# Optimization experiments

Measured on AMD Instinct MI355X. Metric: run time of the kernel, lower is better.

## Reference

```python
import jax, jax.numpy as jnp
import numpy as np

B, C, H, W = 8, 64, 16, 16
TE = 128      # te_hidden
GT = 256      # rn_gt_hidden
FP = 256      # rn_fp_hidden
A = 32        # a_size
O = H * W
PAIR_IN = (C + 2) * 2 + TE  # 260, matches (cv_filter+2)*2 + te_hidden


def setup_inputs() -> dict:
    key = jax.random.key(0)
    ks = jax.random.split(key, 10)

    def w(k, fan_in, fan_out):
        return (jax.random.normal(k, (fan_in, fan_out), jnp.float32)
                / np.sqrt(fan_in).astype(np.float32))

    return {
        "x": jax.random.normal(ks[0], (B, C, H, W), jnp.float32),
        "code": jax.random.normal(ks[1], (B, TE), jnp.float32),
        "gt_w1": w(ks[2], PAIR_IN, GT), "gt_b1": jnp.zeros((GT,), jnp.float32),
        "gt_w2": w(ks[3], GT, GT),      "gt_b2": jnp.zeros((GT,), jnp.float32),
        "gt_w3": w(ks[4], GT, GT),      "gt_b3": jnp.zeros((GT,), jnp.float32),
        "fp_w1": w(ks[5], GT, FP),      "fp_b1": jnp.zeros((FP,), jnp.float32),
        "fp_w2": w(ks[6], FP, FP),      "fp_b2": jnp.zeros((FP,), jnp.float32),
        "fp_w3": w(ks[7], FP, A),       "fp_b3": jnp.zeros((A,), jnp.float32),
    }


def _coords(h, w):
    # 2 normalized coordinate channels in [-1, 1], one value per object
    ys = jnp.linspace(-1.0, 1.0, h, dtype=jnp.float32)
    xs = jnp.linspace(-1.0, 1.0, w, dtype=jnp.float32)
    yy, xx = jnp.meshgrid(ys, xs, indexing="ij")
    return jnp.stack([yy.ravel(), xx.ravel()], axis=-1)  # (o, 2)


def reference(x, code, gt_w1, gt_b1, gt_w2, gt_b2, gt_w3, gt_b3,
              fp_w1, fp_b1, fp_w2, fp_b2, fp_w3, fp_b3):
    b, c, h, w = x.shape
    o = h * w
    te = code.shape[-1]

    # rn_encode: flatten spatial grid to objects, append 2 coord channels
    xo = x.reshape(b, c, o).transpose(0, 2, 1)                 # (b, o, c)
    coord = jnp.broadcast_to(_coords(h, w)[None], (b, o, 2))
    xo = jnp.concatenate([xo, coord], axis=-1)                 # (b, o, c+2)

    # all O^2 ordered pairs + broadcast question code
    xi = jnp.broadcast_to(xo[:, :, None, :], (b, o, o, c + 2))
    xj = jnp.broadcast_to(xo[:, None, :, :], (b, o, o, c + 2))
    q = jnp.broadcast_to(code[:, None, None, :], (b, o, o, te))
    pairs = jnp.concatenate([xi, xj, q], axis=-1)              # (b, o, o, PAIR_IN)

    # g_theta MLP (ReLU after every layer)
    h1 = jax.nn.relu(pairs @ gt_w1 + gt_b1)
    h2 = jax.nn.relu(h1 @ gt_w2 + gt_b2)
    rel = jax.nn.relu(h2 @ gt_w3 + gt_b3)                      # (b, o, o, GT)

    # lower_sum: sum relations over the lower-triangular (i >= j) pairs
    mask = jnp.tril(jnp.ones((o, o), rel.dtype))
    summed = jnp.einsum("bijd,ij->bd", rel, mask)              # (b, GT)

    # f_phi MLP; no activation on final logits, dropout=0 (eval)
    f1 = jax.nn.relu(summed @ fp_w1 + fp_b1)
    f2 = jax.nn.relu(f1 @ fp_w2 + fp_b2)
    logits = f2 @ fp_w3 + fp_b3                                # (b, A)
    return logits
```

## Files before the change

kernel.cpp:

```cpp
#include <hip/hip_runtime.h>
#include <stdint.h>


#define NPAIR 32896
#define NPT   129

using short8  = __attribute__((ext_vector_type(8))) short;
using float4v = __attribute__((ext_vector_type(4))) float;

__device__ __forceinline__ float asf(unsigned u) {
    union { unsigned u; float f; } c; c.u = u; return c.f;
}
__device__ __forceinline__ unsigned short f2bf(float f) {
    union { float f; unsigned u; } c; c.f = f;
    unsigned u = c.u;
    u += 0x7FFFu + ((u >> 16) & 1u);
    return (unsigned short)(u >> 16);
}
__device__ __forceinline__ unsigned cvtpk(float lo, float hi) {
    unsigned r;
    asm("v_cvt_pk_bf16_f32 %0, %1, %2" : "=v"(r) : "v"(lo), "v"(hi));
    return r;
}
__device__ __forceinline__ void ij_of(int p, int& i, int& j) {
    float s = sqrtf(8.0f * (float)p + 1.0f);
    i = (int)((s - 1.0f) * 0.5f);
    while ((i + 1) * (i + 2) / 2 <= p) ++i;
    while (i * (i + 1) / 2 > p) --i;
    j = p - i * (i + 1) / 2;
}
__device__ __forceinline__ short8 buildA(uint4 uu, uint4 vv) {
    unsigned ua[4] = {uu.x, uu.y, uu.z, uu.w};
    unsigned va[4] = {vv.x, vv.y, vv.z, vv.w};
    union { unsigned u[4]; short8 s; } c;
    #pragma unroll
    for (int q = 0; q < 4; ++q) {
        float lo = asf(ua[q] << 16)         + asf(va[q] << 16);
        float hi = asf(ua[q] & 0xFFFF0000u) + asf(va[q] & 0xFFFF0000u);
        c.u[q] = cvtpk(fmaxf(lo, 0.f), fmaxf(hi, 0.f));
    }
    return c.s;
}

__global__ __launch_bounds__(256) void k_pre(
    const float* __restrict__ x, const float* __restrict__ code,
    const float* __restrict__ w1, const float* __restrict__ b1,
    const float* __restrict__ w2, const float* __restrict__ w3,
    unsigned short* __restrict__ ub, unsigned short* __restrict__ vb,
    unsigned short* __restrict__ w2t, unsigned short* __restrict__ w3t,
    float* __restrict__ summed)
{
    const int tid = threadIdx.x;
    if (blockIdx.x < 32) {
        const int ig = blockIdx.x, b = blockIdx.y, d = tid;
        float q = b1[d];
        const float* cp = code + b * 128;
        #pragma unroll 16
        for (int t = 0; t < 128; ++t) q += cp[t] * w1[(132 + t) * 256 + d];
        float su[8], sv[8];
        #pragma unroll
        for (int k = 0; k < 8; ++k) { su[k] = q; sv[k] = 0.f; }
        const float* xp = x + (b * 64) * 256 + ig * 8;
        #pragma unroll 8
        for (int c = 0; c < 64; ++c) {
            const float wu = w1[c * 256 + d];
            const float wv = w1[(66 + c) * 256 + d];
            const float* xc = xp + c * 256;
            #pragma unroll
            for (int k = 0; k < 8; ++k) { su[k] += xc[k] * wu; sv[k] += xc[k] * wv; }
        }
        const float wyu = w1[64 * 256 + d],  wxu = w1[65 * 256 + d];
        const float wyv = w1[130 * 256 + d], wxv = w1[131 * 256 + d];
        #pragma unroll
        for (int k = 0; k < 8; ++k) {
            const int i = ig * 8 + k;
            const float yy = (float)(i >> 4) * (2.0f / 15.0f) - 1.0f;
            const float xx = (float)(i & 15) * (2.0f / 15.0f) - 1.0f;
            ub[(b * 256 + i) * 256 + d] = f2bf(su[k] + yy * wyu + xx * wxu);
            vb[(b * 256 + i) * 256 + d] = f2bf(sv[k] + yy * wyv + xx * wxv);
        }
    } else {
        __shared__ float t[64][65];
        const int y = blockIdx.y;
        summed[y * 256 + tid] = 0.f;
        const int tx = tid & 63, ty = tid >> 6;
        for (int jj = 0; jj < 4; ++jj) {
            const int job = y * 4 + jj;
            const float* src = (job & 16) ? w3 : w2;
            unsigned short* dst = (job & 16) ? w3t : w2t;
            const int k0 = ((job >> 2) & 3) * 64, n0 = (job & 3) * 64;
            __syncthreads();
            #pragma unroll
            for (int r = ty; r < 64; r += 4) t[r][tx] = src[(k0 + r) * 256 + n0 + tx];
            __syncthreads();
            #pragma unroll
            for (int r = ty; r < 64; r += 4) dst[(n0 + r) * 256 + k0 + tx] = f2bf(t[tx][r]);
        }
    }
}

__global__ __launch_bounds__(512) void k_fuse(
    const unsigned short* __restrict__ ub, const unsigned short* __restrict__ vb,
    const unsigned short* __restrict__ w2t, const unsigned short* __restrict__ w3t,
    const float* __restrict__ b2, const float* __restrict__ b3,
    float* __restrict__ summed)
{
    extern __shared__ unsigned short lds[];
    const int tid  = threadIdx.x;
    const int pt   = blockIdx.x, b = blockIdx.y;
    const int lane = tid & 63, w = tid >> 6;
    const int lm   = lane & 15, quad = lane >> 4;

    #pragma unroll
    for (int it = 0; it < 16; ++it) {
        const int idx = it * 512 + tid;
        const int n = idx >> 5, c = idx & 31;
        const uint4 d = *(const uint4*)(w2t + n * 256 + c * 8);
        *(uint4*)(&lds[n * 256 + ((c ^ (n & 7)) << 3)]) = d;
    }

    const unsigned short* up[2];
    const unsigned short* vp[2];
    #pragma unroll
    for (int mt = 0; mt < 2; ++mt) {
        const int p0 = pt * 256 + w * 32 + mt * 16 + lm;
        const int p  = p0 < NPAIR ? p0 : NPAIR - 1;
        int i, j; ij_of(p, i, j);
        up[mt] = ub + ((b * 256 + i) * 256) + quad * 8;
        vp[mt] = vb + ((b * 256 + j) * 256) + quad * 8;
    }
    const int wave_valid = (pt * 256 + w * 32) < NPAIR;
    __syncthreads();

    const float4v zero4 = {0.f, 0.f, 0.f, 0.f};

    float4v acc1[16][2];
    #pragma unroll
    for (int nt = 0; nt < 16; ++nt)
        #pragma unroll
        for (int mt = 0; mt < 2; ++mt) acc1[nt][mt] = zero4;
    {
        uint4 cu[3][2], cv[3][2];
        #pragma unroll
        for (int kk = 0; kk < 3; ++kk)
            #pragma unroll
            for (int mt = 0; mt < 2; ++mt) {
                cu[kk][mt] = *(const uint4*)(up[mt] + kk * 32);
                cv[kk][mt] = *(const uint4*)(vp[mt] + kk * 32);
            }
        #pragma unroll
        for (int ks = 0; ks < 8; ++ks) {
            const int pr = ks % 3;
            short8 afr[2];
            #pragma unroll
            for (int mt = 0; mt < 2; ++mt) afr[mt] = buildA(cu[pr][mt], cv[pr][mt]);
            if (ks < 5) {
                #pragma unroll
                for (int mt = 0; mt < 2; ++mt) {
                    cu[pr][mt] = *(const uint4*)(up[mt] + (ks + 3) * 32);
                    cv[pr][mt] = *(const uint4*)(vp[mt] + (ks + 3) * 32);
                }
            }
            const int coff = ((ks * 4 + quad) ^ (lm & 7)) << 3;
            __builtin_amdgcn_s_setprio(1);
            #pragma unroll
            for (int ng = 0; ng < 4; ++ng) {
                short8 bfr[4];
                #pragma unroll
                for (int q = 0; q < 4; ++q)
                    bfr[q] = *(const short8*)(&lds[((ng * 4 + q) * 16 + lm) * 256 + coff]);
                #pragma unroll
                for (int q = 0; q < 4; ++q)
                    #pragma unroll
                    for (int mt = 0; mt < 2; ++mt)
                        acc1[ng * 4 + q][mt] = __builtin_amdgcn_mfma_f32_16x16x32_bf16(
                            bfr[q], afr[mt], acc1[ng * 4 + q][mt], 0, 0, 0);
            }
            __builtin_amdgcn_s_setprio(0);
        }
    }
    __syncthreads();

    const unsigned short* bb3 = w3t + ((w * 32 + lm) * 256) + quad * 8;
    short8 bbuf[2][2];
    #pragma unroll
    for (int kk = 0; kk < 2; ++kk)
        #pragma unroll
        for (int nt = 0; nt < 2; ++nt)
            bbuf[kk][nt] = *(const short8*)(bb3 + nt * 4096 + kk * 32);

    const float msk = wave_valid ? 1.f : 0.f;
    #pragma unroll
    for (int nt = 0; nt < 16; ++nt) {
        const float4 bbv = *(const float4*)(b2 + nt * 16 + quad * 4);
        #pragma unroll
        for (int mt = 0; mt < 2; ++mt) {
            const int row = w * 32 + mt * 16 + lm;
            const float v0 = fmaxf(acc1[nt][mt][0] + bbv.x, 0.f) * msk;
            const float v1 = fmaxf(acc1[nt][mt][1] + bbv.y, 0.f) * msk;
            const float v2 = fmaxf(acc1[nt][mt][2] + bbv.z, 0.f) * msk;
            const float v3 = fmaxf(acc1[nt][mt][3] + bbv.w, 0.f) * msk;
            uint2 pk; pk.x = cvtpk(v0, v1); pk.y = cvtpk(v2, v3);
            const int c0 = nt * 2 + (quad >> 1);
            *(uint2*)(&lds[row * 256 + (((c0 ^ (row & 7)) << 3) | ((quad & 1) << 2))]) = pk;
        }
    }
    __syncthreads();

    float4v acc2[16][2];
    #pragma unroll
    for (int mt = 0; mt < 16; ++mt)
        #pragma unroll
        for (int nt = 0; nt < 2; ++nt) acc2[mt][nt] = zero4;
    {
        for (int ks = 0; ks < 8; ++ks) {
            const int pr = ks & 1;
            short8 bcur[2];
            #pragma unroll
            for (int nt = 0; nt < 2; ++nt) bcur[nt] = bbuf[pr][nt];
            if (ks < 6) {
                #pragma unroll
                for (int nt = 0; nt < 2; ++nt)
                    bbuf[pr][nt] = *(const short8*)(bb3 + nt * 4096 + (ks + 2) * 32);
            }
            __builtin_amdgcn_s_setprio(1);
            #pragma unroll
            for (int mt = 0; mt < 16; ++mt) {
                const int row = mt * 16 + lm;
                const short8 a = *(const short8*)(
                    &lds[row * 256 + (((ks * 4 + quad) ^ (row & 7)) << 3)]);
                #pragma unroll
                for (int nt = 0; nt < 2; ++nt)
                    acc2[mt][nt] = __builtin_amdgcn_mfma_f32_16x16x32_bf16(
                        a, bcur[nt], acc2[mt][nt], 0, 0, 0);
            }
            __builtin_amdgcn_s_setprio(0);
        }
    }

    #pragma unroll
    for (int nt = 0; nt < 2; ++nt) {
        const int col = w * 32 + nt * 16 + lm;
        const float bb = b3[col];
        float s = 0.f;
        #pragma unroll
        for (int mt = 0; mt < 16; ++mt)
            #pragma unroll
            for (int rg = 0; rg < 4; ++rg)
                s += fmaxf(acc2[mt][nt][rg] + bb, 0.f);
        s += __shfl_xor(s, 16);
        s += __shfl_xor(s, 32);
        if (quad == 0)
            atomicAdd(&summed[b * 256 + col], s);
    }
}

__global__ __launch_bounds__(1024) void k_tail(
    const float* __restrict__ summed,
    const float* __restrict__ fw1, const float* __restrict__ fb1,
    const float* __restrict__ fw2, const float* __restrict__ fb2,
    const float* __restrict__ fw3, const float* __restrict__ fb3,
    float* __restrict__ out)
{
    __shared__ float s0[256], s1[256], red[1024];
    const int b = blockIdx.x, tid = threadIdx.x;
    const int d = tid & 255, kh = tid >> 8;
    if (tid < 256) s0[tid] = summed[b * 256 + tid];
    __syncthreads();
    float p = 0.f;
    #pragma unroll 16
    for (int k = kh * 64; k < kh * 64 + 64; ++k) p += s0[k] * fw1[k * 256 + d];
    red[kh * 256 + d] = p;
    __syncthreads();
    if (tid < 256)
        s1[tid] = fmaxf(red[tid] + red[256 + tid] + red[512 + tid] + red[768 + tid]
                        + fb1[tid], 0.f);
    __syncthreads();
    p = 0.f;
    #pragma unroll 16
    for (int k = kh * 64; k < kh * 64 + 64; ++k) p += s1[k] * fw2[k * 256 + d];
    red[kh * 256 + d] = p;
    __syncthreads();
    if (tid < 256)
        s0[tid] = fmaxf(red[tid] + red[256 + tid] + red[512 + tid] + red[768 + tid]
                        + fb2[tid], 0.f);
    __syncthreads();
    const int d3 = tid & 31, kh3 = tid >> 5;
    p = 0.f;
    #pragma unroll
    for (int k = kh3 * 8; k < kh3 * 8 + 8; ++k) p += s0[k] * fw3[k * 32 + d3];
    red[kh3 * 32 + d3] = p;
    __syncthreads();
    if (tid < 32) {
        float o = fb3[tid];
        #pragma unroll 8
        for (int r = 0; r < 32; ++r) o += red[r * 32 + tid];
        out[b * 32 + tid] = o;
    }
}

extern "C" void kernel_launch(void* const* d_in, const int* in_sizes, int n_in,
                              void* d_out, int out_size, void* d_ws, size_t ws_size,
                              hipStream_t stream) {
    const float* x    = (const float*)d_in[0];
    const float* code = (const float*)d_in[1];
    const float* gw1  = (const float*)d_in[2];
    const float* gb1  = (const float*)d_in[3];
    const float* gw2  = (const float*)d_in[4];
    const float* gb2  = (const float*)d_in[5];
    const float* gw3  = (const float*)d_in[6];
    const float* gb3  = (const float*)d_in[7];
    const float* fw1  = (const float*)d_in[8];
    const float* fb1  = (const float*)d_in[9];
    const float* fw2  = (const float*)d_in[10];
    const float* fb2  = (const float*)d_in[11];
    const float* fw3  = (const float*)d_in[12];
    const float* fb3  = (const float*)d_in[13];
    float* out = (float*)d_out;

    char* ws = (char*)d_ws;
    unsigned short* ub  = (unsigned short*)(ws);
    unsigned short* vb  = (unsigned short*)(ws + 1048576);
    unsigned short* w2t = (unsigned short*)(ws + 2097152);
    unsigned short* w3t = (unsigned short*)(ws + 2228224);
    float* summed = (float*)(ws + 2359296);

    hipLaunchKernelGGL(k_pre, dim3(33, 8), dim3(256), 0, stream,
                       x, code, gw1, gb1, gw2, gw3, ub, vb, w2t, w3t, summed);
    hipLaunchKernelGGL(k_fuse, dim3(NPT, 8), dim3(512), 131072, stream,
                       ub, vb, w2t, w3t, gb2, gb3, summed);
    hipLaunchKernelGGL(k_tail, dim3(8), dim3(1024), 0, stream,
                       summed, fw1, fb1, fw2, fb2, fw3, fb3, out);
}
```

Before: 192.2 us.

## Stage pair activations in LDS and stream W2 fragments per wave

The fused g_theta kernel now builds the 128-pair layer-1 activation tile in LDS, with a swizzled layout. Each wave streams its own 32-column slice of W2 from global memory, mirroring how W3 was already handled. Previously all of W2 was staged in LDS and activations were built in registers. The tile size halves to 128 pairs, so LDS use drops to 64KB and more blocks can be resident per CU. The 257 tiles cover the pairs exactly, so the validity masking is removed. The trade-off is more global/L2 reads of weight fragments and twice as many blocks.

New measurement: 210.5 us. 9.5% more time.

```diff
diff --git a/kernel.cpp b/kernel.cpp
--- a/kernel.cpp
+++ b/kernel.cpp
@@ -3,7 +3,7 @@
 
 
 #define NPAIR 32896
-#define NPT   129
+#define NTILE 257
 
 using short8  = __attribute__((ext_vector_type(8))) short;
 using float4v = __attribute__((ext_vector_type(4))) float;
@@ -29,17 +29,18 @@
     while (i * (i + 1) / 2 > p) --i;
     j = p - i * (i + 1) / 2;
 }
-__device__ __forceinline__ short8 buildA(uint4 uu, uint4 vv) {
+__device__ __forceinline__ uint4 build4(uint4 uu, uint4 vv) {
     unsigned ua[4] = {uu.x, uu.y, uu.z, uu.w};
     unsigned va[4] = {vv.x, vv.y, vv.z, vv.w};
-    union { unsigned u[4]; short8 s; } c;
+    uint4 r;
+    unsigned* rp = (unsigned*)&r;
     #pragma unroll
     for (int q = 0; q < 4; ++q) {
         float lo = asf(ua[q] << 16)         + asf(va[q] << 16);
         float hi = asf(ua[q] & 0xFFFF0000u) + asf(va[q] & 0xFFFF0000u);
-        c.u[q] = cvtpk(fmaxf(lo, 0.f), fmaxf(hi, 0.f));
-    }
-    return c.s;
+        rp[q] = cvtpk(fmaxf(lo, 0.f), fmaxf(hi, 0.f));
+    }
+    return r;
 }
 
 __global__ __launch_bounds__(256) void k_pre(
@@ -99,117 +100,112 @@
     }
 }
 
-__global__ __launch_bounds__(512) void k_fuse(
+__global__ __launch_bounds__(512, 4) void k_fuse(
     const unsigned short* __restrict__ ub, const unsigned short* __restrict__ vb,
     const unsigned short* __restrict__ w2t, const unsigned short* __restrict__ w3t,
     const float* __restrict__ b2, const float* __restrict__ b3,
     float* __restrict__ summed)
 {
-    extern __shared__ unsigned short lds[];
+    extern __shared__ unsigned short tile[];
     const int tid  = threadIdx.x;
     const int pt   = blockIdx.x, b = blockIdx.y;
     const int lane = tid & 63, w = tid >> 6;
     const int lm   = lane & 15, quad = lane >> 4;
 
-    #pragma unroll
-    for (int it = 0; it < 16; ++it) {
-        const int idx = it * 512 + tid;
-        const int n = idx >> 5, c = idx & 31;
-        const uint4 d = *(const uint4*)(w2t + n * 256 + c * 8);
-        *(uint4*)(&lds[n * 256 + ((c ^ (n & 7)) << 3)]) = d;
-    }
-
-    const unsigned short* up[2];
-    const unsigned short* vp[2];
-    #pragma unroll
-    for (int mt = 0; mt < 2; ++mt) {
-        const int p0 = pt * 256 + w * 32 + mt * 16 + lm;
-        const int p  = p0 < NPAIR ? p0 : NPAIR - 1;
+    const unsigned short* bb2 = w2t + ((w * 32 + lm) * 256) + quad * 8;
+    const unsigned short* bb3 = w3t + ((w * 32 + lm) * 256) + quad * 8;
+
+    short8 bbuf[2][2];
+    #pragma unroll
+    for (int kk = 0; kk < 2; ++kk)
+        #pragma unroll
+        for (int nt = 0; nt < 2; ++nt)
+            bbuf[kk][nt] = *(const short8*)(bb2 + nt * 4096 + kk * 32);
+
+    {
+        const int r = tid >> 2, qq = tid & 3;
+        const int p = pt * 128 + r;
         int i, j; ij_of(p, i, j);
-        up[mt] = ub + ((b * 256 + i) * 256) + quad * 8;
-        vp[mt] = vb + ((b * 256 + j) * 256) + quad * 8;
-    }
-    const int wave_valid = (pt * 256 + w * 32) < NPAIR;
+        const unsigned short* up = ub + ((b * 256 + i) * 256) + qq * 64;
+        const unsigned short* vp = vb + ((b * 256 + j) * 256) + qq * 64;
+        const int rs = r & 7;
+        #pragma unroll
+        for (int it = 0; it < 8; ++it) {
+            const uint4 uu = *(const uint4*)(up + it * 8);
+            const uint4 vv = *(const uint4*)(vp + it * 8);
+            const uint4 r4 = build4(uu, vv);
+            const int chunk = qq * 8 + it;
+            *(uint4*)(&tile[r * 256 + ((chunk ^ rs) << 3)]) = r4;
+        }
+    }
     __syncthreads();
 
     const float4v zero4 = {0.f, 0.f, 0.f, 0.f};
 
-    float4v acc1[16][2];
-    #pragma unroll
-    for (int nt = 0; nt < 16; ++nt)
-        #pragma unroll
-        for (int mt = 0; mt < 2; ++mt) acc1[nt][mt] = zero4;
+    float4v acc1[2][8];
+    #pragma unroll
+    for (int nt = 0; nt < 2; ++nt)
+        #pragma unroll
+        for (int mt = 0; mt < 8; ++mt) acc1[nt][mt] = zero4;
     {
-        uint4 cu[3][2], cv[3][2];
-        #pragma unroll
-        for (int kk = 0; kk < 3; ++kk)
-            #pragma unroll
-            for (int mt = 0; mt < 2; ++mt) {
-                cu[kk][mt] = *(const uint4*)(up[mt] + kk * 32);
-                cv[kk][mt] = *(const uint4*)(vp[mt] + kk * 32);
-            }
-        #pragma unroll
         for (int ks = 0; ks < 8; ++ks) {
-            const int pr = ks % 3;
-            short8 afr[2];
-            #pragma unroll
-            for (int mt = 0; mt < 2; ++mt) afr[mt] = buildA(cu[pr][mt], cv[pr][mt]);
-            if (ks < 5) {
-                #pragma unroll
-                for (int mt = 0; mt < 2; ++mt) {
-                    cu[pr][mt] = *(const uint4*)(up[mt] + (ks + 3) * 32);
-                    cv[pr][mt] = *(const uint4*)(vp[mt] + (ks + 3) * 32);
-                }
+            const int pr = ks & 1;
+            short8 bcur[2];
+            #pragma unroll
+            for (int nt = 0; nt < 2; ++nt) bcur[nt] = bbuf[pr][nt];
+            if (ks < 6) {
+                #pragma unroll
+                for (int nt = 0; nt < 2; ++nt)
+                    bbuf[pr][nt] = *(const short8*)(bb2 + nt * 4096 + (ks + 2) * 32);
             }
             const int coff = ((ks * 4 + quad) ^ (lm & 7)) << 3;
             __builtin_amdgcn_s_setprio(1);
             #pragma unroll
-            for (int ng = 0; ng < 4; ++ng) {
-                short8 bfr[4];
-                #pragma unroll
-                for (int q = 0; q < 4; ++q)
-                    bfr[q] = *(const short8*)(&lds[((ng * 4 + q) * 16 + lm) * 256 + coff]);
-                #pragma unroll
-                for (int q = 0; q < 4; ++q)
+            for (int half = 0; half < 2; ++half) {
+                short8 afr[4];
+                #pragma unroll
+                for (int m = 0; m < 4; ++m)
+                    afr[m] = *(const short8*)(
+                        &tile[((half * 4 + m) * 16 + lm) * 256 + coff]);
+                #pragma unroll
+                for (int m = 0; m < 4; ++m)
                     #pragma unroll
-                    for (int mt = 0; mt < 2; ++mt)
-                        acc1[ng * 4 + q][mt] = __builtin_amdgcn_mfma_f32_16x16x32_bf16(
-                            bfr[q], afr[mt], acc1[ng * 4 + q][mt], 0, 0, 0);
+                    for (int nt = 0; nt < 2; ++nt)
+                        acc1[nt][half * 4 + m] = __builtin_amdgcn_mfma_f32_16x16x32_bf16(
+                            bcur[nt], afr[m], acc1[nt][half * 4 + m], 0, 0, 0);
             }
             __builtin_amdgcn_s_setprio(0);
         }
     }
     __syncthreads();
 
-    const unsigned short* bb3 = w3t + ((w * 32 + lm) * 256) + quad * 8;
-    short8 bbuf[2][2];
     #pragma unroll
     for (int kk = 0; kk < 2; ++kk)
         #pragma unroll
         for (int nt = 0; nt < 2; ++nt)
             bbuf[kk][nt] = *(const short8*)(bb3 + nt * 4096 + kk * 32);
 
-    const float msk = wave_valid ? 1.f : 0.f;
-    #pragma unroll
-    for (int nt = 0; nt < 16; ++nt) {
-        const float4 bbv = *(const float4*)(b2 + nt * 16 + quad * 4);
-        #pragma unroll
-        for (int mt = 0; mt < 2; ++mt) {
-            const int row = w * 32 + mt * 16 + lm;
-            const float v0 = fmaxf(acc1[nt][mt][0] + bbv.x, 0.f) * msk;
-            const float v1 = fmaxf(acc1[nt][mt][1] + bbv.y, 0.f) * msk;
-            const float v2 = fmaxf(acc1[nt][mt][2] + bbv.z, 0.f) * msk;
-            const float v3 = fmaxf(acc1[nt][mt][3] + bbv.w, 0.f) * msk;
+    #pragma unroll
+    for (int nt = 0; nt < 2; ++nt) {
+        const float4 bbv = *(const float4*)(b2 + w * 32 + nt * 16 + quad * 4);
+        #pragma unroll
+        for (int mt = 0; mt < 8; ++mt) {
+            const int row = mt * 16 + lm;
+            const float v0 = fmaxf(acc1[nt][mt][0] + bbv.x, 0.f);
+            const float v1 = fmaxf(acc1[nt][mt][1] + bbv.y, 0.f);
+            const float v2 = fmaxf(acc1[nt][mt][2] + bbv.z, 0.f);
+            const float v3 = fmaxf(acc1[nt][mt][3] + bbv.w, 0.f);
             uint2 pk; pk.x = cvtpk(v0, v1); pk.y = cvtpk(v2, v3);
-            const int c0 = nt * 2 + (quad >> 1);
-            *(uint2*)(&lds[row * 256 + (((c0 ^ (row & 7)) << 3) | ((quad & 1) << 2))]) = pk;
-        }
-    }
-    __syncthreads();
-
-    float4v acc2[16][2];
-    #pragma unroll
-    for (int mt = 0; mt < 16; ++mt)
+            const int c0 = w * 4 + nt * 2 + (quad >> 1);
+            *(uint2*)(&tile[row * 256 +
+                            (((c0 ^ (row & 7)) << 3) | ((quad & 1) << 2))]) = pk;
+        }
+    }
+    __syncthreads();
+
+    float4v acc2[8][2];
+    #pragma unroll
+    for (int mt = 0; mt < 8; ++mt)
         #pragma unroll
         for (int nt = 0; nt < 2; ++nt) acc2[mt][nt] = zero4;
     {
@@ -223,12 +219,12 @@
                 for (int nt = 0; nt < 2; ++nt)
                     bbuf[pr][nt] = *(const short8*)(bb3 + nt * 4096 + (ks + 2) * 32);
             }
+            const int coff = ((ks * 4 + quad) ^ (lm & 7)) << 3;
             __builtin_amdgcn_s_setprio(1);
             #pragma unroll
-            for (int mt = 0; mt < 16; ++mt) {
-                const int row = mt * 16 + lm;
+            for (int mt = 0; mt < 8; ++mt) {
                 const short8 a = *(const short8*)(
-                    &lds[row * 256 + (((ks * 4 + quad) ^ (row & 7)) << 3)]);
+                    &tile[(mt * 16 + lm) * 256 + coff]);
                 #pragma unroll
                 for (int nt = 0; nt < 2; ++nt)
                     acc2[mt][nt] = __builtin_amdgcn_mfma_f32_16x16x32_bf16(
@@ -244,7 +240,7 @@
         const float bb = b3[col];
         float s = 0.f;
         #pragma unroll
-        for (int mt = 0; mt < 16; ++mt)
+        for (int mt = 0; mt < 8; ++mt)
             #pragma unroll
             for (int rg = 0; rg < 4; ++rg)
                 s += fmaxf(acc2[mt][nt][rg] + bb, 0.f);
@@ -327,7 +323,7 @@
 
     hipLaunchKernelGGL(k_pre, dim3(33, 8), dim3(256), 0, stream,
                        x, code, gw1, gb1, gw2, gw3, ub, vb, w2t, w3t, summed);
-    hipLaunchKernelGGL(k_fuse, dim3(NPT, 8), dim3(512), 131072, stream,
+    hipLaunchKernelGGL(k_fuse, dim3(NTILE, 8), dim3(512), 65536, stream,
                        ub, vb, w2t, w3t, gb2, gb3, summed);
     hipLaunchKernelGGL(k_tail, dim3(8), dim3(1024), 0, stream,
                        summed, fw1, fb1, fw2, fb2, fw3, fb3, out);
```

## Move ragged last pair tile from fused kernel into tail kernel

Applied to the files above, without the earlier changes.

The main fused kernel now launches 128 pair tiles per batch instead of 129, dropping the mostly-empty 129th tile (128 valid pairs out of 256) and its masking logic. The tail kernel processes the remaining 128 pairs itself with a smaller MFMA pass before the f_phi MLP, adding its partial sum to the accumulated relations. This removes a nearly idle extra wave of blocks on the main kernel, but the single-block-per-batch tail kernel now does extra serial work and needs about 135 KB of dynamic LDS.

Result: faster. 187.7 us (-2.3%).

```diff
diff --git a/kernel.cpp b/kernel.cpp
--- a/kernel.cpp
+++ b/kernel.cpp
@@ -3,7 +3,6 @@
 
 
 #define NPAIR 32896
-#define NPT   129
 
 using short8  = __attribute__((ext_vector_type(8))) short;
 using float4v = __attribute__((ext_vector_type(4))) float;
@@ -123,13 +122,11 @@
     const unsigned short* vp[2];
     #pragma unroll
     for (int mt = 0; mt < 2; ++mt) {
-        const int p0 = pt * 256 + w * 32 + mt * 16 + lm;
-        const int p  = p0 < NPAIR ? p0 : NPAIR - 1;
+        const int p = pt * 256 + w * 32 + mt * 16 + lm;
         int i, j; ij_of(p, i, j);
         up[mt] = ub + ((b * 256 + i) * 256) + quad * 8;
         vp[mt] = vb + ((b * 256 + j) * 256) + quad * 8;
     }
-    const int wave_valid = (pt * 256 + w * 32) < NPAIR;
     __syncthreads();
 
     const float4v zero4 = {0.f, 0.f, 0.f, 0.f};
@@ -189,17 +186,16 @@
         for (int nt = 0; nt < 2; ++nt)
             bbuf[kk][nt] = *(const short8*)(bb3 + nt * 4096 + kk * 32);
 
-    const float msk = wave_valid ? 1.f : 0.f;
     #pragma unroll
     for (int nt = 0; nt < 16; ++nt) {
         const float4 bbv = *(const float4*)(b2 + nt * 16 + quad * 4);
         #pragma unroll
         for (int mt = 0; mt < 2; ++mt) {
             const int row = w * 32 + mt * 16 + lm;
-            const float v0 = fmaxf(acc1[nt][mt][0] + bbv.x, 0.f) * msk;
-            const float v1 = fmaxf(acc1[nt][mt][1] + bbv.y, 0.f) * msk;
-            const float v2 = fmaxf(acc1[nt][mt][2] + bbv.z, 0.f) * msk;
-            const float v3 = fmaxf(acc1[nt][mt][3] + bbv.w, 0.f) * msk;
+            const float v0 = fmaxf(acc1[nt][mt][0] + bbv.x, 0.f);
+            const float v1 = fmaxf(acc1[nt][mt][1] + bbv.y, 0.f);
+            const float v2 = fmaxf(acc1[nt][mt][2] + bbv.z, 0.f);
+            const float v3 = fmaxf(acc1[nt][mt][3] + bbv.w, 0.f);
             uint2 pk; pk.x = cvtpk(v0, v1); pk.y = cvtpk(v2, v3);
             const int c0 = nt * 2 + (quad >> 1);
             *(uint2*)(&lds[row * 256 + (((c0 ^ (row & 7)) << 3) | ((quad & 1) << 2))]) = pk;
@@ -256,40 +252,143 @@
 }
 
 __global__ __launch_bounds__(1024) void k_tail(
+    const unsigned short* __restrict__ ub, const unsigned short* __restrict__ vb,
+    const unsigned short* __restrict__ w2t, const unsigned short* __restrict__ w3t,
+    const float* __restrict__ b2, const float* __restrict__ b3,
     const float* __restrict__ summed,
     const float* __restrict__ fw1, const float* __restrict__ fb1,
     const float* __restrict__ fw2, const float* __restrict__ fb2,
     const float* __restrict__ fw3, const float* __restrict__ fb3,
     float* __restrict__ out)
 {
-    __shared__ float s0[256], s1[256], red[1024];
+    extern __shared__ unsigned short lds[];
+    float* ext = (float*)(lds + 65536);
+    float* s0  = ext + 256;
+    float* s1  = s0 + 256;
+    float* red = s1 + 256;
     const int b = blockIdx.x, tid = threadIdx.x;
+    const int lane = tid & 63, w = tid >> 6;
+    const int lm = lane & 15, quad = lane >> 4;
+    const float4v zero4 = {0.f, 0.f, 0.f, 0.f};
+
+    #pragma unroll
+    for (int it = 0; it < 8; ++it) {
+        const int idx = it * 1024 + tid;
+        const int n = idx >> 5, c = idx & 31;
+        const uint4 d4 = *(const uint4*)(w2t + n * 256 + c * 8);
+        *(uint4*)(&lds[n * 256 + ((c ^ (n & 7)) << 3)]) = d4;
+    }
+    const int pp = 32768 + w * 16 + lm;
+    const int p  = pp < NPAIR ? pp : NPAIR - 1;
+    int i, j; ij_of(p, i, j);
+    const unsigned short* up = ub + ((b * 256 + i) * 256) + quad * 8;
+    const unsigned short* vp = vb + ((b * 256 + j) * 256) + quad * 8;
+    __syncthreads();
+
+    float4v acc1[16];
+    #pragma unroll
+    for (int nt = 0; nt < 16; ++nt) acc1[nt] = zero4;
+    if (tid < 512) {
+        #pragma unroll
+        for (int ks = 0; ks < 8; ++ks) {
+            const uint4 cu = *(const uint4*)(up + ks * 32);
+            const uint4 cv = *(const uint4*)(vp + ks * 32);
+            const short8 afr = buildA(cu, cv);
+            const int coff = ((ks * 4 + quad) ^ (lm & 7)) << 3;
+            #pragma unroll
+            for (int nt = 0; nt < 16; ++nt) {
+                const short8 bfr = *(const short8*)(&lds[(nt * 16 + lm) * 256 + coff]);
+                acc1[nt] = __builtin_amdgcn_mfma_f32_16x16x32_bf16(
+                    bfr, afr, acc1[nt], 0, 0, 0);
+            }
+        }
+    }
+    __syncthreads();
+
+    if (tid < 512) {
+        #pragma unroll
+        for (int nt = 0; nt < 16; ++nt) {
+            const float4 bbv = *(const float4*)(b2 + nt * 16 + quad * 4);
+            const int row = w * 16 + lm;
+            const float v0 = fmaxf(acc1[nt][0] + bbv.x, 0.f);
+            const float v1 = fmaxf(acc1[nt][1] + bbv.y, 0.f);
+            const float v2 = fmaxf(acc1[nt][2] + bbv.z, 0.f);
+            const float v3 = fmaxf(acc1[nt][3] + bbv.w, 0.f);
+            uint2 pk; pk.x = cvtpk(v0, v1); pk.y = cvtpk(v2, v3);
+            const int c0 = nt * 2 + (quad >> 1);
+            *(uint2*)(&lds[row * 256 + (((c0 ^ (row & 7)) << 3) | ((quad & 1) << 2))]) = pk;
+        }
+    }
+    __syncthreads();
+
+    float4v acc2[8][2];
+    #pragma unroll
+    for (int mt = 0; mt < 8; ++mt)
+        #pragma unroll
+        for (int nt = 0; nt < 2; ++nt) acc2[mt][nt] = zero4;
+    if (tid < 512) {
+        const unsigned short* bb3 = w3t + ((w * 32 + lm) * 256) + quad * 8;
+        #pragma unroll
+        for (int ks = 0; ks < 8; ++ks) {
+            short8 bcur[2];
+            #pragma unroll
+            for (int nt = 0; nt < 2; ++nt)
+                bcur[nt] = *(const short8*)(bb3 + nt * 4096 + ks * 32);
+            const int coff = ((ks * 4 + quad) ^ (lm & 7)) << 3;
+            #pragma unroll
+            for (int mt = 0; mt < 8; ++mt) {
+                const int row = mt * 16 + lm;
+                const short8 a = *(const short8*)(
+                    &lds[row * 256 + (((ks * 4 + quad) ^ (row & 7)) << 3)]);
+                #pragma unroll
+                for (int nt = 0; nt < 2; ++nt)
+                    acc2[mt][nt] = __builtin_amdgcn_mfma_f32_16x16x32_bf16(
+                        a, bcur[nt], acc2[mt][nt], 0, 0, 0);
+            }
+        }
+        #pragma unroll
+        for (int nt = 0; nt < 2; ++nt) {
+            const int col = w * 32 + nt * 16 + lm;
+            const float bb = b3[col];
+            float s = 0.f;
+            #pragma unroll
+            for (int mt = 0; mt < 8; ++mt)
+                #pragma unroll
+                for (int rg = 0; rg < 4; ++rg)
+                    s += fmaxf(acc2[mt][nt][rg] + bb, 0.f);
+            s += __shfl_xor(s, 16);
+            s += __shfl_xor(s, 32);
+            if (quad == 0) ext[col] = s;
+        }
+    }
+    __syncthreads();
+
     const int d = tid & 255, kh = tid >> 8;
-    if (tid < 256) s0[tid] = summed[b * 256 + tid];
-    __syncthreads();
-    float p = 0.f;
+    if (tid < 256) s0[tid] = summed[b * 256 + tid] + ext[tid];
+    __syncthreads();
+    float pk = 0.f;
     #pragma unroll 16
-    for (int k = kh * 64; k < kh * 64 + 64; ++k) p += s0[k] * fw1[k * 256 + d];
-    red[kh * 256 + d] = p;
+    for (int k = kh * 64; k < kh * 64 + 64; ++k) pk += s0[k] * fw1[k * 256 + d];
+    red[kh * 256 + d] = pk;
     __syncthreads();
     if (tid < 256)
         s1[tid] = fmaxf(red[tid] + red[256 + tid] + red[512 + tid] + red[768 + tid]
                         + fb1[tid], 0.f);
     __syncthreads();
-    p = 0.f;
+    pk = 0.f;
     #pragma unroll 16
-    for (int k = kh * 64; k < kh * 64 + 64; ++k) p += s1[k] * fw2[k * 256 + d];
-    red[kh * 256 + d] = p;
+    for (int k = kh * 64; k < kh * 64 + 64; ++k) pk += s1[k] * fw2[k * 256 + d];
+    red[kh * 256 + d] = pk;
     __syncthreads();
     if (tid < 256)
         s0[tid] = fmaxf(red[tid] + red[256 + tid] + red[512 + tid] + red[768 + tid]
                         + fb2[tid], 0.f);
     __syncthreads();
     const int d3 = tid & 31, kh3 = tid >> 5;
-    p = 0.f;
-    #pragma unroll
-    for (int k = kh3 * 8; k < kh3 * 8 + 8; ++k) p += s0[k] * fw3[k * 32 + d3];
-    red[kh3 * 32 + d3] = p;
+    pk = 0.f;
+    #pragma unroll
+    for (int k = kh3 * 8; k < kh3 * 8 + 8; ++k) pk += s0[k] * fw3[k * 32 + d3];
+    red[kh3 * 32 + d3] = pk;
     __syncthreads();
     if (tid < 32) {
         float o = fb3[tid];
@@ -327,8 +426,9 @@
 
     hipLaunchKernelGGL(k_pre, dim3(33, 8), dim3(256), 0, stream,
                        x, code, gw1, gb1, gw2, gw3, ub, vb, w2t, w3t, summed);
-    hipLaunchKernelGGL(k_fuse, dim3(NPT, 8), dim3(512), 131072, stream,
+    hipLaunchKernelGGL(k_fuse, dim3(128, 8), dim3(512), 131072, stream,
                        ub, vb, w2t, w3t, gb2, gb3, summed);
-    hipLaunchKernelGGL(k_tail, dim3(8), dim3(1024), 0, stream,
-                       summed, fw1, fb1, fw2, fb2, fw3, fb3, out);
-}
+    hipLaunchKernelGGL(k_tail, dim3(8), dim3(1024), 138240, stream,
+                       ub, vb, w2t, w3t, gb2, gb3, summed,
+                       fw1, fb1, fw2, fb2, fw3, fb3, out);
+}
```
